# Optimization experiments

Measured on AMD Instinct MI355X. Metric: run time of the kernel, lower is better.

Reference implementation:

```python
import jax, jax.numpy as jnp
import numpy as np

DIM = 256
HEADS = 8
H = 56
W = 56
WS = 7          # window size
SHIFT = 3       # cyclic shift
MLP_HIDDEN = 4 * DIM
HEAD_DIM = DIM // HEADS
SCALE = HEAD_DIM ** -0.5
N = WS * WS     # tokens per window
EPS = 1e-5


def _rel_pos_index():
    coords = np.stack(np.meshgrid(np.arange(WS), np.arange(WS), indexing='ij'))  # [2,ws,ws]
    cf = coords.reshape(2, -1)                       # [2, N]
    rel = cf[:, :, None] - cf[:, None, :]            # [2, N, N]
    rel = rel.transpose(1, 2, 0).copy()              # [N, N, 2]
    rel[:, :, 0] += WS - 1
    rel[:, :, 1] += WS - 1
    rel[:, :, 1] *= 2 * WS - 1
    return rel.sum(-1)                               # [N, N]

REL_IDX = jnp.asarray(_rel_pos_index())


def _attn_mask():
    # shifted-window attention mask, computed once (static)
    img = np.zeros((H, W))
    cnt = 0
    slices = (slice(0, -WS), slice(-WS, -SHIFT), slice(-SHIFT, None))
    for hs in slices:
        for ws in slices:
            img[hs, ws] = cnt
            cnt += 1
    mw = img.reshape(H // WS, WS, W // WS, WS).transpose(0, 2, 1, 3).reshape(-1, N)  # [nW, N]
    am = mw[:, None, :] - mw[:, :, None]
    return jnp.asarray(np.where(am != 0, -100.0, 0.0).astype(np.float32))  # [nW, N, N]

ATTN_MASK = _attn_mask()


def _layernorm(y, g, b):
    mu = y.mean(-1, keepdims=True)
    var = ((y - mu) ** 2).mean(-1, keepdims=True)
    return (y - mu) * jax.lax.rsqrt(var + EPS) * g + b


def setup_inputs() -> dict:
    key = jax.random.key(0)
    ks = jax.random.split(key, 10)
    B = 32
    x = jax.random.normal(ks[0], (B, H * W, DIM), dtype=jnp.float32)
    qkv_w = jax.random.normal(ks[1], (DIM, 3 * DIM), dtype=jnp.float32) * 0.02
    qkv_b = jnp.zeros((3 * DIM,), dtype=jnp.float32)
    proj_w = jax.random.normal(ks[2], (DIM, DIM), dtype=jnp.float32) * 0.02
    proj_b = jnp.zeros((DIM,), dtype=jnp.float32)
    bias_table = jax.random.normal(ks[3], ((2 * WS - 1) * (2 * WS - 1), HEADS), dtype=jnp.float32) * 0.02
    norm1_g = jnp.ones((DIM,), dtype=jnp.float32)
    norm1_b = jnp.zeros((DIM,), dtype=jnp.float32)
    norm2_g = jnp.ones((DIM,), dtype=jnp.float32)
    norm2_b = jnp.zeros((DIM,), dtype=jnp.float32)
    mlp_w1 = jax.random.normal(ks[4], (DIM, MLP_HIDDEN), dtype=jnp.float32) * 0.02
    mlp_b1 = jnp.zeros((MLP_HIDDEN,), dtype=jnp.float32)
    mlp_w2 = jax.random.normal(ks[5], (MLP_HIDDEN, DIM), dtype=jnp.float32) * 0.02
    mlp_b2 = jnp.zeros((DIM,), dtype=jnp.float32)
    return dict(x=x, norm1_g=norm1_g, norm1_b=norm1_b, qkv_w=qkv_w, qkv_b=qkv_b,
                proj_w=proj_w, proj_b=proj_b, bias_table=bias_table,
                norm2_g=norm2_g, norm2_b=norm2_b,
                mlp_w1=mlp_w1, mlp_b1=mlp_b1, mlp_w2=mlp_w2, mlp_b2=mlp_b2)


def reference(x, norm1_g, norm1_b, qkv_w, qkv_b, proj_w, proj_b, bias_table,
              norm2_g, norm2_b, mlp_w1, mlp_b1, mlp_w2, mlp_b2):
    B, M, C = x.shape
    shortcut = x
    y = _layernorm(x, norm1_g, norm1_b).reshape(B, H, W, C)
    # cyclic shift
    y = jnp.roll(y, (-SHIFT, -SHIFT), axis=(1, 2))
    # window partition: [B,H,W,C] -> [B*nW, N, C]
    win = y.reshape(B, H // WS, WS, W // WS, WS, C).transpose(0, 1, 3, 2, 4, 5).reshape(-1, N, C)
    Bw = win.shape[0]
    qkv = (win @ qkv_w + qkv_b).reshape(Bw, N, 3, HEADS, HEAD_DIM).transpose(2, 0, 3, 1, 4)
    q, k, v = qkv[0], qkv[1], qkv[2]               # each [Bw, heads, N, hd]
    attn = jnp.einsum('bhnd,bhmd->bhnm', q, k) * SCALE
    bias = bias_table[REL_IDX].transpose(2, 0, 1)  # [heads, N, N]
    attn = attn + bias[None]
    nW = ATTN_MASK.shape[0]
    attn = attn.reshape(B, nW, HEADS, N, N) + ATTN_MASK[None, :, None]
    attn = jax.nn.softmax(attn.reshape(Bw, HEADS, N, N), axis=-1)
    out = jnp.einsum('bhnm,bhmd->bhnd', attn, v).transpose(0, 2, 1, 3).reshape(Bw, N, C)
    out = out @ proj_w + proj_b
    # window reverse and un-shift
    out = out.reshape(B, H // WS, W // WS, WS, WS, C).transpose(0, 1, 3, 2, 4, 5).reshape(B, H, W, C)
    out = jnp.roll(out, (SHIFT, SHIFT), axis=(1, 2)).reshape(B, M, C)
    x = shortcut + out
    h = _layernorm(x, norm2_g, norm2_b)
    h = jax.nn.gelu(h @ mlp_w1 + mlp_b1) @ mlp_w2 + mlp_b2
    return x + h
```

## Files before the change

### kernel.cpp

```cpp
#include <hip/hip_runtime.h>
#include <hip/hip_bf16.h>
#include <math.h>

typedef __bf16 bf16_t;
typedef __attribute__((ext_vector_type(8))) __bf16 bf16x8;
typedef __attribute__((ext_vector_type(4))) __bf16 bf16x4;
typedef __attribute__((ext_vector_type(4))) float f32x4;

#define T_TOK 100352
#define DIMC 256
#define HEADS 8
#define HD 32
#define NTOK 49
#define SHIFT3 3
#define HH 56
#define SCALE_QK 0.17677669529663687f

__device__ __forceinline__ int xrow_of(int rr) {
    int wi = rr / 49; int t = rr - wi * 49;
    int b = wi >> 6; int w64 = wi & 63;
    int wh = w64 >> 3, ww = w64 & 7;
    int i = t / 7, j = t - i * 7;
    int hy = wh * 7 + i, wy = ww * 7 + j;
    int hx = hy + SHIFT3; if (hx >= HH) hx -= HH;
    int wx = wy + SHIFT3; if (wx >= HH) wx -= HH;
    return b * (HH * HH) + hx * HH + wx;
}

__global__ __launch_bounds__(256) void transpose_cast(const float* __restrict__ W,
                                                      bf16_t* __restrict__ WT,
                                                      int K, int Nc) {
    int t = blockIdx.x * 256 + threadIdx.x;
    int k = t / Nc, c = t - k * Nc;
    WT[(size_t)c * K + k] = (bf16_t)W[t];
}

template <int MAP>
__global__ __launch_bounds__(256) void ln_kernel(const float* __restrict__ x,
                                                 const float* __restrict__ g,
                                                 const float* __restrict__ bsh,
                                                 bf16_t* __restrict__ out) {
    int wv = threadIdx.x >> 6, l = threadIdx.x & 63;
    int r = blockIdx.x * 4 + wv;
    int xr = MAP ? xrow_of(r) : r;
    float4 v = ((const float4*)(x + (size_t)xr * DIMC))[l];
    float s = v.x + v.y + v.z + v.w;
    float sq = v.x * v.x + v.y * v.y + v.z * v.z + v.w * v.w;
    #pragma unroll
    for (int off = 32; off; off >>= 1) {
        s += __shfl_down(s, off);
        sq += __shfl_down(sq, off);
    }
    s = __shfl(s, 0); sq = __shfl(sq, 0);
    float mean = s * (1.f / 256.f);
    float var = sq * (1.f / 256.f) - mean * mean;
    float rstd = rsqrtf(var + 1e-5f);
    float4 gv = ((const float4*)g)[l];
    float4 bv = ((const float4*)bsh)[l];
    bf16x4 o;
    o[0] = (bf16_t)((v.x - mean) * rstd * gv.x + bv.x);
    o[1] = (bf16_t)((v.y - mean) * rstd * gv.y + bv.y);
    o[2] = (bf16_t)((v.z - mean) * rstd * gv.z + bv.z);
    o[3] = (bf16_t)((v.w - mean) * rstd * gv.w + bv.w);
    *(bf16x4*)(out + (size_t)r * DIMC + l * 4) = o;
}

template <int EPI>
__global__ __launch_bounds__(256) void gemm128(const bf16_t* __restrict__ A,
                                               const bf16_t* __restrict__ BT,
                                               const float* __restrict__ bias,
                                               int Nc, int K,
                                               bf16_t* __restrict__ outb,
                                               float* __restrict__ outf,
                                               const float* __restrict__ resid) {
    __shared__ bf16_t As[128 * 32];
    __shared__ bf16_t Bs[128 * 32];
    int tid = threadIdx.x;
    int wv = tid >> 6, l = tid & 63;
    int wr = wv >> 1, wc = wv & 1;
    int nTilesN = Nc >> 7;
    int qn = gridDim.x >> 3;
    int lb = (blockIdx.x & 7) * qn + (blockIdx.x >> 3);
    int bm = lb / nTilesN, bn = lb - bm * nTilesN;
    size_t row0 = (size_t)bm * 128;
    int col0 = bn * 128;

    const char* Abase = (const char*)(A + row0 * K);
    const char* Bbase = (const char*)(BT + (size_t)col0 * K);
    const size_t ldb = (size_t)K * 2;

    f32x4 acc[4][4] = {};
    const int lr = l & 15, lk = (l >> 4) * 8;
    const int aoff = (wr * 64 + lr) * 32 + lk;
    const int boff = (wc * 64 + lr) * 32 + lk;

    for (int kk = 0; kk < K; kk += 32) {
        #pragma unroll
        for (int it = 0; it < 2; ++it) {
            int t = tid + it * 256;
            int row = t >> 2, cb = (t & 3) * 16;
            __builtin_amdgcn_global_load_lds(
                (const __attribute__((address_space(1))) void*)(Abase + (size_t)row * ldb + (size_t)kk * 2 + cb),
                (__attribute__((address_space(3))) void*)((char*)As + t * 16), 16, 0, 0);
            __builtin_amdgcn_global_load_lds(
                (const __attribute__((address_space(1))) void*)(Bbase + (size_t)row * ldb + (size_t)kk * 2 + cb),
                (__attribute__((address_space(3))) void*)((char*)Bs + t * 16), 16, 0, 0);
        }
        __syncthreads();
        bf16x8 a[4], b[4];
        #pragma unroll
        for (int m = 0; m < 4; ++m) a[m] = *(const bf16x8*)(As + aoff + m * 16 * 32);
        #pragma unroll
        for (int n = 0; n < 4; ++n) b[n] = *(const bf16x8*)(Bs + boff + n * 16 * 32);
        #pragma unroll
        for (int m = 0; m < 4; ++m)
            #pragma unroll
            for (int n = 0; n < 4; ++n)
                acc[m][n] = __builtin_amdgcn_mfma_f32_16x16x32_bf16(a[m], b[n], acc[m][n], 0, 0, 0);
        __syncthreads();
    }

    #pragma unroll
    for (int m = 0; m < 4; ++m) {
        #pragma unroll
        for (int i = 0; i < 4; ++i) {
            int rr = (int)row0 + wr * 64 + m * 16 + (l >> 4) * 4 + i;
            size_t orow = (EPI == 3) ? (size_t)xrow_of(rr) * DIMC : (size_t)rr * Nc;
            #pragma unroll
            for (int n = 0; n < 4; ++n) {
                int cc = col0 + wc * 64 + n * 16 + (l & 15);
                float v = acc[m][n][i] + bias[cc];
                if (EPI == 0) {
                    outb[(size_t)rr * Nc + cc] = (bf16_t)v;
                } else if (EPI == 1) {
                    float t3 = v + 0.044715f * v * v * v;
                    float e = __expf(-1.5957691216057308f * t3);
                    float gl = v * __builtin_amdgcn_rcpf(1.f + e);
                    outb[(size_t)rr * Nc + cc] = (bf16_t)gl;
                } else if (EPI == 2) {
                    size_t o = (size_t)rr * Nc + cc;
                    outf[o] = v + resid[o];
                } else {
                    size_t o = orow + cc;
                    outf[o] = v + resid[o];
                }
            }
        }
    }
}

__global__ __launch_bounds__(256) void attn_mfma(const bf16_t* __restrict__ qkv,
                                                 const float* __restrict__ bt,
                                                 bf16_t* __restrict__ out) {
    __shared__ __align__(16) char lds[4][12800];
    int wv = threadIdx.x >> 6, l = threadIdx.x & 63;
    int head = ((blockIdx.x & 1) << 2) | wv;
    int wi = blockIdx.x >> 1;
    char* W = lds[wv];
    bf16_t* Vt = (bf16_t*)(W + 8192);
    size_t rowbase = (size_t)wi * NTOK;
    const bf16_t* src = qkv + rowbase * 768 + head * HD;

    int w64 = wi & 63;
    int wh = w64 >> 3, ww = w64 & 7;
    bool lastH = (wh == 7), lastW = (ww == 7);
    bool masked = lastH || lastW;

    #pragma unroll
    for (int it = 0; it < 4; ++it) {
        int t = l + it * 64;
        int r = t >> 2, g = t & 3;
        if (r < NTOK) {
            bf16x8 qv = *(const bf16x8*)(src + (size_t)r * 768 + g * 8);
            bf16x8 kv = *(const bf16x8*)(src + (size_t)r * 768 + 256 + g * 8);
            int sa = (r * 64 + g * 16) ^ ((r & 7) << 4);
            *(bf16x8*)(W + sa) = qv;
            *(bf16x8*)(W + 4096 + sa) = kv;
        }
    }
    #pragma unroll
    for (int it = 0; it < 4; ++it) {
        int t = l + it * 64;
        int m = t >> 2, dc = t & 3;
        if (m < NTOK) {
            bf16x8 vv = *(const bf16x8*)(src + (size_t)m * 768 + 512 + dc * 8);
            #pragma unroll
            for (int j = 0; j < 8; ++j) Vt[(dc * 8 + j) * 72 + m] = vv[j];
        } else {
            #pragma unroll
            for (int j = 0; j < 8; ++j) Vt[(dc * 8 + j) * 72 + m] = (bf16_t)0.f;
        }
    }

    int lr = l & 15, g4 = l >> 4;

    bf16x8 a[4], b[4];
    #pragma unroll
    for (int mt = 0; mt < 4; ++mt) {
        int r = mt * 16 + lr;
        int sa = (r * 64 + g4 * 16) ^ ((r & 7) << 4);
        a[mt] = *(const bf16x8*)(W + sa);
        b[mt] = *(const bf16x8*)(W + 4096 + sa);
    }
    f32x4 z = {0.f, 0.f, 0.f, 0.f};
    f32x4 S[4][4];
    #pragma unroll
    for (int mt = 0; mt < 4; ++mt)
        #pragma unroll
        for (int nt = 0; nt < 4; ++nt)
            S[mt][nt] = __builtin_amdgcn_mfma_f32_16x16x32_bf16(a[mt], b[nt], z, 0, 0, 0);

    int i2[4], j2[4], reg2[4];
    #pragma unroll
    for (int nt = 0; nt < 4; ++nt) {
        int cm = nt * 16 + lr;
        i2[nt] = (cm * 147) >> 10;
        j2[nt] = cm - i2[nt] * 7;
        int rh = lastH ? ((i2[nt] < 4) ? 1 : 2) : 0;
        int rw = lastW ? ((j2[nt] < 4) ? 1 : 2) : 0;
        reg2[nt] = rh * 3 + rw;
    }

    #pragma unroll
    for (int mt = 0; mt < 4; ++mt) {
        #pragma unroll
        for (int i = 0; i < 4; ++i) {
            int rn = mt * 16 + g4 * 4 + i;
            bool rowok = rn < NTOK;
            int i1 = (rn * 147) >> 10, j1 = rn - i1 * 7;
            int rh1 = lastH ? ((i1 < 4) ? 1 : 2) : 0;
            int rw1 = lastW ? ((j1 < 4) ? 1 : 2) : 0;
            int reg1 = rh1 * 3 + rw1;
            float sv[4];
            #pragma unroll
            for (int nt = 0; nt < 4; ++nt) {
                int cm = nt * 16 + lr;
                float sc;
                if (rowok && cm < NTOK) {
                    sc = S[mt][nt][i] * SCALE_QK;
                    sc += bt[((i1 - i2[nt] + 6) + 13 * (j1 - j2[nt] + 6)) * 8 + head];
                    if (masked && (reg1 != reg2[nt])) sc -= 100.f;
                } else {
                    sc = -1e30f;
                }
                sv[nt] = sc;
            }
            float mx = fmaxf(fmaxf(sv[0], sv[1]), fmaxf(sv[2], sv[3]));
            mx = fmaxf(mx, __shfl_xor(mx, 1));
            mx = fmaxf(mx, __shfl_xor(mx, 2));
            mx = fmaxf(mx, __shfl_xor(mx, 4));
            mx = fmaxf(mx, __shfl_xor(mx, 8));
            float e[4];
            float sum = 0.f;
            #pragma unroll
            for (int nt = 0; nt < 4; ++nt) { e[nt] = __expf(sv[nt] - mx); sum += e[nt]; }
            sum += __shfl_xor(sum, 1);
            sum += __shfl_xor(sum, 2);
            sum += __shfl_xor(sum, 4);
            sum += __shfl_xor(sum, 8);
            float inv = 1.f / sum;
            #pragma unroll
            for (int nt = 0; nt < 4; ++nt) {
                int cm = nt * 16 + lr;
                int pa = (rn * 128 + cm * 2) ^ ((rn & 7) << 4);
                *(bf16_t*)(W + pa) = (bf16_t)(e[nt] * inv);
            }
        }
    }

    f32x4 o[4][2] = {};
    #pragma unroll
    for (int ks = 0; ks < 2; ++ks) {
        bf16x8 pa[4], vb[2];
        #pragma unroll
        for (int mt = 0; mt < 4; ++mt) {
            int r = mt * 16 + lr;
            int ad = (r * 128 + ks * 64 + g4 * 16) ^ ((r & 7) << 4);
            pa[mt] = *(const bf16x8*)(W + ad);
        }
        #pragma unroll
        for (int dt = 0; dt < 2; ++dt) {
            int d = dt * 16 + lr;
            vb[dt] = *(const bf16x8*)((char*)Vt + d * 144 + ks * 64 + g4 * 16);
        }
        #pragma unroll
        for (int mt = 0; mt < 4; ++mt)
            #pragma unroll
            for (int dt = 0; dt < 2; ++dt)
                o[mt][dt] = __builtin_amdgcn_mfma_f32_16x16x32_bf16(pa[mt], vb[dt], o[mt][dt], 0, 0, 0);
    }

    #pragma unroll
    for (int mt = 0; mt < 4; ++mt) {
        #pragma unroll
        for (int i = 0; i < 4; ++i) {
            int n = mt * 16 + g4 * 4 + i;
            if (n < NTOK) {
                #pragma unroll
                for (int dt = 0; dt < 2; ++dt) {
                    out[(rowbase + n) * DIMC + head * HD + dt * 16 + lr] = (bf16_t)o[mt][dt][i];
                }
            }
        }
    }
}

extern "C" void kernel_launch(void* const* d_in, const int* in_sizes, int n_in,
                              void* d_out, int out_size, void* d_ws, size_t ws_size,
                              hipStream_t stream) {
    const float* x      = (const float*)d_in[0];
    const float* n1g    = (const float*)d_in[1];
    const float* n1b    = (const float*)d_in[2];
    const float* qkv_w  = (const float*)d_in[3];
    const float* qkv_b  = (const float*)d_in[4];
    const float* proj_w = (const float*)d_in[5];
    const float* proj_b = (const float*)d_in[6];
    const float* btab   = (const float*)d_in[7];
    const float* n2g    = (const float*)d_in[8];
    const float* n2b    = (const float*)d_in[9];
    const float* w1     = (const float*)d_in[10];
    const float* b1     = (const float*)d_in[11];
    const float* w2     = (const float*)d_in[12];
    const float* b2     = (const float*)d_in[13];

    char* ws = (char*)d_ws;
    bf16_t* win      = (bf16_t*)(ws);
    bf16_t* qkvbuf   = (bf16_t*)(ws + (size_t)T_TOK * 256 * 2);
    bf16_t* mlp1_buf = (bf16_t*)(ws);
    bf16_t* h2       = (bf16_t*)(ws + (size_t)T_TOK * 2048);
    char* wtp        = ws + (size_t)T_TOK * 2048 + (size_t)T_TOK * 512;
    bf16_t* wt_qkv   = (bf16_t*)wtp;
    bf16_t* wt_proj  = wt_qkv + 768 * 256;
    bf16_t* wt_mlp1  = wt_proj + 256 * 256;
    bf16_t* wt_mlp2  = wt_mlp1 + 1024 * 256;
    float* xmid      = (float*)d_out;

    transpose_cast<<<768, 256, 0, stream>>>(qkv_w, wt_qkv, 256, 768);
    transpose_cast<<<256, 256, 0, stream>>>(proj_w, wt_proj, 256, 256);
    transpose_cast<<<1024, 256, 0, stream>>>(w1, wt_mlp1, 256, 1024);
    transpose_cast<<<1024, 256, 0, stream>>>(w2, wt_mlp2, 1024, 256);

    ln_kernel<1><<<T_TOK / 4, 256, 0, stream>>>(x, n1g, n1b, win);
    gemm128<0><<<(T_TOK / 128) * (768 / 128), 256, 0, stream>>>(win, wt_qkv, qkv_b, 768, 256,
                                                                qkvbuf, nullptr, nullptr);
    attn_mfma<<<2048 * 2, 256, 0, stream>>>(qkvbuf, btab, win);
    gemm128<3><<<(T_TOK / 128) * (256 / 128), 256, 0, stream>>>(win, wt_proj, proj_b, 256, 256,
                                                                nullptr, xmid, x);
    ln_kernel<0><<<T_TOK / 4, 256, 0, stream>>>(xmid, n2g, n2b, h2);
    gemm128<1><<<(T_TOK / 128) * (1024 / 128), 256, 0, stream>>>(h2, wt_mlp1, b1, 1024, 256,
                                                                 mlp1_buf, nullptr, nullptr);
    gemm128<2><<<(T_TOK / 128) * (256 / 128), 256, 0, stream>>>(mlp1_buf, wt_mlp2, b2, 256, 1024,
                                                                nullptr, xmid, xmid);
}
```

Measured before the change: 585.4 us.

## Double-buffer GEMM LDS tiles with 64-wide K, XOR swizzle, and async prefetch

Rewrites the bf16 GEMM main loop to use two LDS buffers of 128x64 tiles. The next K-slice is loaded asynchronously with global_load_lds while MFMAs run on the current one, and partial vmcnt waits replace full syncs. LDS chunks are XOR-swizzled by row to avoid bank conflicts on the bf16x8 fragment reads. K becomes a template parameter so the loop fully unrolls, and setprio is raised around the MFMA bursts. LDS use per block quadruples to 64KB, which may reduce occupancy.

```diff
diff --git a/kernel.cpp b/kernel.cpp
--- a/kernel.cpp
+++ b/kernel.cpp
@@ -65,16 +65,17 @@
     *(bf16x4*)(out + (size_t)r * DIMC + l * 4) = o;
 }
 
-template <int EPI>
+template <int EPI, int KT>
 __global__ __launch_bounds__(256) void gemm128(const bf16_t* __restrict__ A,
                                                const bf16_t* __restrict__ BT,
                                                const float* __restrict__ bias,
-                                               int Nc, int K,
+                                               int Nc,
                                                bf16_t* __restrict__ outb,
                                                float* __restrict__ outf,
                                                const float* __restrict__ resid) {
-    __shared__ bf16_t As[128 * 32];
-    __shared__ bf16_t Bs[128 * 32];
+    constexpr int NS = KT / 64;
+    __shared__ bf16_t As[2][128 * 64];
+    __shared__ bf16_t Bs[2][128 * 64];
     int tid = threadIdx.x;
     int wv = tid >> 6, l = tid & 63;
     int wr = wv >> 1, wc = wv & 1;
@@ -85,50 +86,75 @@
     size_t row0 = (size_t)bm * 128;
     int col0 = bn * 128;
 
-    const char* Abase = (const char*)(A + row0 * K);
-    const char* Bbase = (const char*)(BT + (size_t)col0 * K);
-    const size_t ldb = (size_t)K * 2;
+    const char* Abase = (const char*)(A + row0 * KT);
+    const char* Bbase = (const char*)(BT + (size_t)col0 * KT);
+    const size_t ldb = (size_t)KT * 2;
+
+    auto STAGE = [&](int buf, int kk) {
+        #pragma unroll
+        for (int it = 0; it < 4; ++it) {
+            int ci = tid + it * 256;
+            int row = ci >> 3, ch = ci & 7;
+            int sc = ch ^ (row & 7);
+            __builtin_amdgcn_global_load_lds(
+                (const __attribute__((address_space(1))) void*)(Abase + (size_t)row * ldb + (size_t)kk * 2 + sc * 16),
+                (__attribute__((address_space(3))) void*)((char*)As[buf] + ci * 16), 16, 0, 0);
+            __builtin_amdgcn_global_load_lds(
+                (const __attribute__((address_space(1))) void*)(Bbase + (size_t)row * ldb + (size_t)kk * 2 + sc * 16),
+                (__attribute__((address_space(3))) void*)((char*)Bs[buf] + ci * 16), 16, 0, 0);
+        }
+    };
 
     f32x4 acc[4][4] = {};
-    const int lr = l & 15, lk = (l >> 4) * 8;
-    const int aoff = (wr * 64 + lr) * 32 + lk;
-    const int boff = (wc * 64 + lr) * 32 + lk;
-
-    for (int kk = 0; kk < K; kk += 32) {
-        #pragma unroll
-        for (int it = 0; it < 2; ++it) {
-            int t = tid + it * 256;
-            int row = t >> 2, cb = (t & 3) * 16;
-            __builtin_amdgcn_global_load_lds(
-                (const __attribute__((address_space(1))) void*)(Abase + (size_t)row * ldb + (size_t)kk * 2 + cb),
-                (__attribute__((address_space(3))) void*)((char*)As + t * 16), 16, 0, 0);
-            __builtin_amdgcn_global_load_lds(
-                (const __attribute__((address_space(1))) void*)(Bbase + (size_t)row * ldb + (size_t)kk * 2 + cb),
-                (__attribute__((address_space(3))) void*)((char*)Bs + t * 16), 16, 0, 0);
-        }
-        __syncthreads();
-        bf16x8 a[4], b[4];
-        #pragma unroll
-        for (int m = 0; m < 4; ++m) a[m] = *(const bf16x8*)(As + aoff + m * 16 * 32);
-        #pragma unroll
-        for (int n = 0; n < 4; ++n) b[n] = *(const bf16x8*)(Bs + boff + n * 16 * 32);
-        #pragma unroll
-        for (int m = 0; m < 4; ++m)
-            #pragma unroll
-            for (int n = 0; n < 4; ++n)
-                acc[m][n] = __builtin_amdgcn_mfma_f32_16x16x32_bf16(a[m], b[n], acc[m][n], 0, 0, 0);
-        __syncthreads();
+    const int lr = l & 15, g4 = l >> 4;
+
+    STAGE(0, 0);
+    if (NS > 1) STAGE(1, 64);
+
+    #pragma unroll
+    for (int s = 0; s < NS; ++s) {
+        if (s + 1 < NS) { asm volatile("s_waitcnt vmcnt(8)" ::: "memory"); }
+        else            { asm volatile("s_waitcnt vmcnt(0)" ::: "memory"); }
+        __builtin_amdgcn_s_barrier();
+        __builtin_amdgcn_sched_barrier(0);
+        int buf = s & 1;
+        #pragma unroll
+        for (int ks = 0; ks < 2; ++ks) {
+            bf16x8 a[4], b[4];
+            #pragma unroll
+            for (int mt = 0; mt < 4; ++mt) {
+                int rr = wr * 64 + mt * 16 + lr;
+                int c = (ks * 4 + g4) ^ (rr & 7);
+                a[mt] = *(const bf16x8*)((char*)As[buf] + rr * 128 + c * 16);
+            }
+            #pragma unroll
+            for (int nt = 0; nt < 4; ++nt) {
+                int rc = wc * 64 + nt * 16 + lr;
+                int c = (ks * 4 + g4) ^ (rc & 7);
+                b[nt] = *(const bf16x8*)((char*)Bs[buf] + rc * 128 + c * 16);
+            }
+            __builtin_amdgcn_s_setprio(1);
+            #pragma unroll
+            for (int mt = 0; mt < 4; ++mt)
+                #pragma unroll
+                for (int nt = 0; nt < 4; ++nt)
+                    acc[mt][nt] = __builtin_amdgcn_mfma_f32_16x16x32_bf16(a[mt], b[nt], acc[mt][nt], 0, 0, 0);
+            __builtin_amdgcn_s_setprio(0);
+        }
+        __builtin_amdgcn_s_barrier();
+        __builtin_amdgcn_sched_barrier(0);
+        if (s + 2 < NS) STAGE(buf, (s + 2) * 64);
     }
 
     #pragma unroll
     for (int m = 0; m < 4; ++m) {
         #pragma unroll
         for (int i = 0; i < 4; ++i) {
-            int rr = (int)row0 + wr * 64 + m * 16 + (l >> 4) * 4 + i;
+            int rr = (int)row0 + wr * 64 + m * 16 + g4 * 4 + i;
             size_t orow = (EPI == 3) ? (size_t)xrow_of(rr) * DIMC : (size_t)rr * Nc;
             #pragma unroll
             for (int n = 0; n < 4; ++n) {
-                int cc = col0 + wc * 64 + n * 16 + (l & 15);
+                int cc = col0 + wc * 64 + n * 16 + lr;
                 float v = acc[m][n][i] + bias[cc];
                 if (EPI == 0) {
                     outb[(size_t)rr * Nc + cc] = (bf16_t)v;
@@ -341,14 +367,14 @@
     transpose_cast<<<1024, 256, 0, stream>>>(w2, wt_mlp2, 1024, 256);
 
     ln_kernel<1><<<T_TOK / 4, 256, 0, stream>>>(x, n1g, n1b, win);
-    gemm128<0><<<(T_TOK / 128) * (768 / 128), 256, 0, stream>>>(win, wt_qkv, qkv_b, 768, 256,
-                                                                qkvbuf, nullptr, nullptr);
+    gemm128<0, 256><<<(T_TOK / 128) * (768 / 128), 256, 0, stream>>>(win, wt_qkv, qkv_b, 768,
+                                                                     qkvbuf, nullptr, nullptr);
     attn_mfma<<<2048 * 2, 256, 0, stream>>>(qkvbuf, btab, win);
-    gemm128<3><<<(T_TOK / 128) * (256 / 128), 256, 0, stream>>>(win, wt_proj, proj_b, 256, 256,
-                                                                nullptr, xmid, x);
+    gemm128<3, 256><<<(T_TOK / 128) * (256 / 128), 256, 0, stream>>>(win, wt_proj, proj_b, 256,
+                                                                     nullptr, xmid, x);
     ln_kernel<0><<<T_TOK / 4, 256, 0, stream>>>(xmid, n2g, n2b, h2);
-    gemm128<1><<<(T_TOK / 128) * (1024 / 128), 256, 0, stream>>>(h2, wt_mlp1, b1, 1024, 256,
-                                                                 mlp1_buf, nullptr, nullptr);
-    gemm128<2><<<(T_TOK / 128) * (256 / 128), 256, 0, stream>>>(mlp1_buf, wt_mlp2, b2, 256, 1024,
-                                                                nullptr, xmid, xmid);
-}
+    gemm128<1, 256><<<(T_TOK / 128) * (1024 / 128), 256, 0, stream>>>(h2, wt_mlp1, b1, 1024,
+                                                                      mlp1_buf, nullptr, nullptr);
+    gemm128<2, 1024><<<(T_TOK / 128) * (256 / 128), 256, 0, stream>>>(mlp1_buf, wt_mlp2, b2, 256,
+                                                                      nullptr, xmid, xmid);
+}
```

New measurement: 547.0 us. 6.6% less time.
